# Optimization experiments

Measured on AMD Instinct MI355X. Metric: run time of the kernel, lower is better.

The kernel has to match this reference:

```python
import jax, jax.numpy as jnp
import numpy as np

EMBED_DIM = 2048
NUM_HEADS = 32
NUM_KV_HEADS = 8
HEAD_DIM = EMBED_DIM // NUM_HEADS  # 64
KV_DIM = NUM_KV_HEADS * HEAD_DIM   # 512


def setup_inputs() -> dict:
    key = jax.random.key(0)
    ks = jax.random.split(key, 5)
    B, S = 2, 2048
    scale = 0.02
    x = jax.random.normal(ks[0], (B, S, EMBED_DIM), dtype=jnp.float32)
    Wq = jax.random.normal(ks[1], (EMBED_DIM, EMBED_DIM), dtype=jnp.float32) * scale
    Wk = jax.random.normal(ks[2], (EMBED_DIM, KV_DIM), dtype=jnp.float32) * scale
    Wv = jax.random.normal(ks[3], (EMBED_DIM, KV_DIM), dtype=jnp.float32) * scale
    Wo = jax.random.normal(ks[4], (EMBED_DIM, EMBED_DIM), dtype=jnp.float32) * scale
    return {"x": x, "Wq": Wq, "Wk": Wk, "Wv": Wv, "Wo": Wo}


def reference(x, Wq, Wk, Wv, Wo):
    B, S, _ = x.shape
    g = NUM_HEADS // NUM_KV_HEADS  # queries per kv head
    # projections -> [B, H, S, D]
    q = (x @ Wq).reshape(B, S, NUM_HEADS, HEAD_DIM).transpose(0, 2, 1, 3)
    k = (x @ Wk).reshape(B, S, NUM_KV_HEADS, HEAD_DIM).transpose(0, 2, 1, 3)
    v = (x @ Wv).reshape(B, S, NUM_KV_HEADS, HEAD_DIM).transpose(0, 2, 1, 3)
    # GQA repeat_interleave on head dim
    k = jnp.repeat(k, g, axis=1)
    v = jnp.repeat(v, g, axis=1)
    scores = jnp.einsum('bhqd,bhkd->bhqk', q, k) / np.sqrt(HEAD_DIM).astype(np.float32)
    causal = jnp.tril(jnp.ones((S, S), dtype=bool))
    scores = jnp.where(causal, scores, jnp.finfo(x.dtype).min)
    attn = jax.nn.softmax(scores, axis=-1)
    out = jnp.einsum('bhqk,bhkd->bhqd', attn, v)  # [B, H, S, D]
    out = out.transpose(0, 2, 1, 3).reshape(B, S, EMBED_DIM)
    return out @ Wo
```

## Files before the change

### kernel.cpp

```cpp
#include <hip/hip_runtime.h>
#include <hip/hip_bf16.h>
#include <cstdint>
#include <type_traits>

#define EMBED 2048
#define SLEN 2048
#define NB 2
#define NHEADS 32
#define HDIM 64
#define KVDIM 512
#define MTOT (NB * SLEN)
#define NQKV (EMBED + 2 * KVDIM)

typedef __attribute__((ext_vector_type(8))) __bf16 bf16x8;
typedef __attribute__((ext_vector_type(4))) float f32x4;
typedef __attribute__((ext_vector_type(16))) float f32x16;

#define QSCALE 0.18033688011112042f

__device__ __forceinline__ ushort f2bf(float f) {
    union { float f; uint32_t u; } v; v.f = f;
    uint32_t r = (v.u + 0x7FFFu + ((v.u >> 16) & 1u)) >> 16;
    return (ushort)r;
}

__device__ __forceinline__ void gload_lds16(const ushort* g, ushort* l) {
    __builtin_amdgcn_global_load_lds(
        (const __attribute__((address_space(1))) void*)g,
        (__attribute__((address_space(3))) void*)l, 16, 0, 0);
}

__global__ __launch_bounds__(256) void k_prep(const float* __restrict__ x,
                                              const float* __restrict__ Wq,
                                              const float* __restrict__ Wk,
                                              const float* __restrict__ Wv,
                                              const float* __restrict__ Wo,
                                              ushort* __restrict__ xb,
                                              ushort* __restrict__ wt,
                                              ushort* __restrict__ wot) {
    const int tid = threadIdx.x;
    int bid = blockIdx.x;
    if (bid < 8192) {
        int i = bid * 256 + tid;
        float4 v = *(const float4*)(x + (size_t)i * 4);
        ushort4 o;
        o.x = f2bf(v.x); o.y = f2bf(v.y); o.z = f2bf(v.z); o.w = f2bf(v.w);
        *(ushort4*)(xb + (size_t)i * 4) = o;
        return;
    }
    bid -= 8192;
    const float* W; ushort* Wt; int N; float scale; int bx, by;
    if (bid < 4096)      { W = Wq; Wt = wt;                                   N = EMBED; scale = QSCALE; bx = bid & 63; by = bid >> 6; }
    else if (bid < 5120) { W = Wk; Wt = wt + (size_t)EMBED * EMBED;           N = KVDIM; scale = 1.f; int b2 = bid - 4096; bx = b2 & 15; by = b2 >> 4; }
    else if (bid < 6144) { W = Wv; Wt = wt + (size_t)(EMBED + KVDIM) * EMBED; N = KVDIM; scale = 1.f; int b2 = bid - 5120; bx = b2 & 15; by = b2 >> 4; }
    else                 { W = Wo; Wt = wot;                                  N = EMBED; scale = 1.f; int b2 = bid - 6144; bx = b2 & 63; by = b2 >> 6; }
    const int K = EMBED;
    __shared__ float tile[32][33];
    const int tx = tid & 31, ty = tid >> 5;
    const int xcol = bx * 32 + tx;
    const int y0 = by * 32;
    #pragma unroll
    for (int i = ty; i < 32; i += 8)
        tile[i][tx] = W[(size_t)(y0 + i) * N + xcol];
    __syncthreads();
    const int xo = y0 + tx;
    const int yo0 = bx * 32;
    #pragma unroll
    for (int i = ty; i < 32; i += 8)
        Wt[(size_t)(yo0 + i) * K + xo] = f2bf(tile[tx][i] * scale);
}

__global__ __launch_bounds__(256) void k_gemm_qkv2(const ushort* __restrict__ A,
                                                   const ushort* __restrict__ WtAll,
                                                   ushort* __restrict__ Qb,
                                                   ushort* __restrict__ Kb,
                                                   ushort* __restrict__ VT) {
    __shared__ alignas(16) ushort As[2][128 * 64];
    __shared__ alignas(16) ushort Bs[2][128 * 64];

    const int tid = threadIdx.x;
    const int lane = tid & 63;
    const int w = tid >> 6;
    const int wr = w >> 1, wc = w & 1;
    const int l15 = lane & 15, g = lane >> 4;
    const int K = EMBED;
    const int bid = blockIdx.x;

    if (bid < 512) {
        int f = (bid & 7) * 64 + (bid >> 3);
        const int bx = f % (EMBED / 128), by = f / (EMBED / 128);
        const int n0 = bx * 128, m0 = by * 128;
        const ushort* Bt = WtAll;

        f32x4 acc[4][4] = {};
        const ushort* pA[4];
        const ushort* pB[4];
        #pragma unroll
        for (int t = 0; t < 4; t++) {
            const int c = tid + 256 * t;
            const int r = c >> 3, gr = c & 7;
            const int sg = gr ^ (r & 7);
            pA[t] = A + (size_t)(m0 + r) * K + sg * 8;
            pB[t] = Bt + (size_t)(n0 + r) * K + sg * 8;
        }
        #pragma unroll
        for (int t = 0; t < 4; t++) {
            gload_lds16(pA[t], &As[0][(tid + 256 * t) * 8]);
            gload_lds16(pB[t], &Bs[0][(tid + 256 * t) * 8]);
        }
        __syncthreads();

        int cur = 0;
        for (int k0 = 0; k0 < K; k0 += 64) {
            if (k0 + 64 < K) {
                #pragma unroll
                for (int t = 0; t < 4; t++) {
                    gload_lds16(pA[t] + k0 + 64, &As[cur ^ 1][(tid + 256 * t) * 8]);
                    gload_lds16(pB[t] + k0 + 64, &Bs[cur ^ 1][(tid + 256 * t) * 8]);
                }
            }
            #pragma unroll
            for (int kk = 0; kk < 2; kk++) {
                bf16x8 a[4], b[4];
                #pragma unroll
                for (int i = 0; i < 4; i++)
                    a[i] = *(const bf16x8*)&As[cur][(wr * 64 + i * 16 + l15) * 64 +
                                                    (((4 * kk + g) ^ (l15 & 7)) << 3)];
                #pragma unroll
                for (int j = 0; j < 4; j++)
                    b[j] = *(const bf16x8*)&Bs[cur][(wc * 64 + j * 16 + l15) * 64 +
                                                    (((4 * kk + g) ^ (l15 & 7)) << 3)];
                #pragma unroll
                for (int i = 0; i < 4; i++)
                    #pragma unroll
                    for (int j = 0; j < 4; j++)
                        acc[i][j] = __builtin_amdgcn_mfma_f32_16x16x32_bf16(a[i], b[j], acc[i][j], 0, 0, 0);
            }
            __syncthreads();
            cur ^= 1;
        }
        #pragma unroll
        for (int i = 0; i < 4; i++)
            #pragma unroll
            for (int j = 0; j < 4; j++) {
                const int row = m0 + wr * 64 + i * 16 + g * 4;
                const int col = n0 + wc * 64 + j * 16 + l15;
                #pragma unroll
                for (int r = 0; r < 4; r++)
                    Qb[(size_t)(row + r) * EMBED + col] = f2bf(acc[i][j][r]);
            }
    } else {
        int f0 = bid - 512;
        int f = (f0 & 7) * 64 + (f0 >> 3);
        const int bx = f % 8, by = f / 8;
        const int n0 = bx * 128, m0 = by * 64;
        const ushort* Bt = WtAll + (size_t)EMBED * EMBED;

        f32x4 acc[2][4] = {};
        const ushort* pA[2];
        const ushort* pB[4];
        #pragma unroll
        for (int t = 0; t < 2; t++) {
            const int c = tid + 256 * t;
            const int r = c >> 3, gr = c & 7;
            const int sg = gr ^ (r & 7);
            pA[t] = A + (size_t)(m0 + r) * K + sg * 8;
        }
        #pragma unroll
        for (int t = 0; t < 4; t++) {
            const int c = tid + 256 * t;
            const int r = c >> 3, gr = c & 7;
            const int sg = gr ^ (r & 7);
            pB[t] = Bt + (size_t)(n0 + r) * K + sg * 8;
        }
        #pragma unroll
        for (int t = 0; t < 2; t++)
            gload_lds16(pA[t], &As[0][(tid + 256 * t) * 8]);
        #pragma unroll
        for (int t = 0; t < 4; t++)
            gload_lds16(pB[t], &Bs[0][(tid + 256 * t) * 8]);
        __syncthreads();

        int cur = 0;
        for (int k0 = 0; k0 < K; k0 += 64) {
            if (k0 + 64 < K) {
                #pragma unroll
                for (int t = 0; t < 2; t++)
                    gload_lds16(pA[t] + k0 + 64, &As[cur ^ 1][(tid + 256 * t) * 8]);
                #pragma unroll
                for (int t = 0; t < 4; t++)
                    gload_lds16(pB[t] + k0 + 64, &Bs[cur ^ 1][(tid + 256 * t) * 8]);
            }
            #pragma unroll
            for (int kk = 0; kk < 2; kk++) {
                bf16x8 a[2], b[4];
                #pragma unroll
                for (int i = 0; i < 2; i++)
                    a[i] = *(const bf16x8*)&As[cur][(wr * 32 + i * 16 + l15) * 64 +
                                                    (((4 * kk + g) ^ (l15 & 7)) << 3)];
                #pragma unroll
                for (int j = 0; j < 4; j++)
                    b[j] = *(const bf16x8*)&Bs[cur][(wc * 64 + j * 16 + l15) * 64 +
                                                    (((4 * kk + g) ^ (l15 & 7)) << 3)];
                #pragma unroll
                for (int i = 0; i < 2; i++)
                    #pragma unroll
                    for (int j = 0; j < 4; j++)
                        acc[i][j] = __builtin_amdgcn_mfma_f32_16x16x32_bf16(a[i], b[j], acc[i][j], 0, 0, 0);
            }
            __syncthreads();
            cur ^= 1;
        }

        if (n0 < KVDIM) {
            #pragma unroll
            for (int i = 0; i < 2; i++)
                #pragma unroll
                for (int j = 0; j < 4; j++) {
                    const int row = m0 + wr * 32 + i * 16 + g * 4;
                    const int col = n0 + wc * 64 + j * 16 + l15;
                    #pragma unroll
                    for (int r = 0; r < 4; r++)
                        Kb[(size_t)(row + r) * KVDIM + col] = f2bf(acc[i][j][r]);
                }
        } else {
            ushort* TT = &Bs[0][0];
            #pragma unroll
            for (int i = 0; i < 2; i++)
                #pragma unroll
                for (int j = 0; j < 4; j++) {
                    const int rowL = wr * 32 + i * 16 + g * 4;
                    const int colL = wc * 64 + j * 16 + l15;
                    #pragma unroll
                    for (int r = 0; r < 4; r++)
                        TT[colL * 72 + rowL + r] = f2bf(acc[i][j][r]);
                }
            __syncthreads();
            const int c = tid >> 1, half = tid & 1;
            const ushort* src = TT + c * 72 + half * 32;
            ushort* dst = VT + (size_t)(n0 - KVDIM + c) * MTOT + m0 + half * 32;
            #pragma unroll
            for (int q = 0; q < 4; q++)
                *(uint4*)(dst + q * 8) = *(const uint4*)(src + q * 8);
        }
    }
}

template <typename OUT_T>
__global__ __launch_bounds__(256) void k_gemm_bt(const ushort* __restrict__ A,
                                                 const ushort* __restrict__ Bt,
                                                 OUT_T* __restrict__ C,
                                                 int M, int N, int K) {
    __shared__ alignas(16) ushort As[2][128 * 64];
    __shared__ alignas(16) ushort Bs[2][128 * 64];

    const int tid = threadIdx.x;
    const int lane = tid & 63;
    const int w = tid >> 6;
    const int wr = w >> 1, wc = w & 1;
    const int l15 = lane & 15, g = lane >> 4;
    const int nwg = (N / 128) * (M / 128);
    int f = blockIdx.y * (N / 128) + blockIdx.x;
    f = (f & 7) * (nwg >> 3) + (f >> 3);
    const int n0 = (f % (N / 128)) * 128;
    const int m0 = (f / (N / 128)) * 128;

    f32x4 acc[4][4] = {};

    const ushort* pA[4];
    const ushort* pB[4];
    #pragma unroll
    for (int t = 0; t < 4; t++) {
        const int c = tid + 256 * t;
        const int r = c >> 3, gr = c & 7;
        const int sg = gr ^ (r & 7);
        pA[t] = A + (size_t)(m0 + r) * K + sg * 8;
        pB[t] = Bt + (size_t)(n0 + r) * K + sg * 8;
    }

    #pragma unroll
    for (int t = 0; t < 4; t++) {
        gload_lds16(pA[t], &As[0][(tid + 256 * t) * 8]);
        gload_lds16(pB[t], &Bs[0][(tid + 256 * t) * 8]);
    }
    __syncthreads();

    int cur = 0;
    for (int k0 = 0; k0 < K; k0 += 64) {
        if (k0 + 64 < K) {
            #pragma unroll
            for (int t = 0; t < 4; t++) {
                gload_lds16(pA[t] + k0 + 64, &As[cur ^ 1][(tid + 256 * t) * 8]);
                gload_lds16(pB[t] + k0 + 64, &Bs[cur ^ 1][(tid + 256 * t) * 8]);
            }
        }
        #pragma unroll
        for (int kk = 0; kk < 2; kk++) {
            bf16x8 a[4], b[4];
            #pragma unroll
            for (int i = 0; i < 4; i++)
                a[i] = *(const bf16x8*)&As[cur][(wr * 64 + i * 16 + l15) * 64 +
                                                (((4 * kk + g) ^ (l15 & 7)) << 3)];
            #pragma unroll
            for (int j = 0; j < 4; j++)
                b[j] = *(const bf16x8*)&Bs[cur][(wc * 64 + j * 16 + l15) * 64 +
                                                (((4 * kk + g) ^ (l15 & 7)) << 3)];
            #pragma unroll
            for (int i = 0; i < 4; i++)
                #pragma unroll
                for (int j = 0; j < 4; j++)
                    acc[i][j] = __builtin_amdgcn_mfma_f32_16x16x32_bf16(a[i], b[j], acc[i][j], 0, 0, 0);
        }
        __syncthreads();
        cur ^= 1;
    }

    #pragma unroll
    for (int i = 0; i < 4; i++) {
        #pragma unroll
        for (int j = 0; j < 4; j++) {
            const int row = m0 + wr * 64 + i * 16 + g * 4;
            const int col = n0 + wc * 64 + j * 16 + l15;
            #pragma unroll
            for (int r = 0; r < 4; r++) {
                float val = acc[i][j][r];
                if constexpr (std::is_same<OUT_T, ushort>::value)
                    C[(size_t)(row + r) * N + col] = f2bf(val);
                else
                    C[(size_t)(row + r) * N + col] = val;
            }
        }
    }
}

__global__ __launch_bounds__(512, 4) void k_attn(const ushort* __restrict__ Qg,
                                                 const ushort* __restrict__ Kg,
                                                 const ushort* __restrict__ VTg,
                                                 ushort* __restrict__ Og) {
    __shared__ alignas(16) ushort Ks[2][64 * 64];
    __shared__ alignas(16) ushort Vs[2][64 * 64];

    const int tid = threadIdx.x;
    const int lane = tid & 63;
    const int wq = tid >> 6;
    const int l31 = lane & 31;
    const int hi = lane >> 5;

    const int flat = blockIdx.x + (blockIdx.y << 3) + (blockIdx.z << 8);
    const int lo = flat & 255, hv = flat >> 8;
    const int bi = hv ? (7 - (lo & 7)) : (lo & 7);
    const int h = lo >> 3;
    const int b = hv;
    const int kh = h >> 2;
    const size_t rowbase = (size_t)b * SLEN;

    const int q0 = bi * 256;
    const int qw0 = q0 + wq * 32;
    const int nt = (q0 >> 6) + 4;

    bf16x8 qf[4];
    {
        const ushort* qrow = Qg + (rowbase + qw0 + l31) * EMBED + h * HDIM;
        #pragma unroll
        for (int s = 0; s < 4; s++)
            qf[s] = *(const bf16x8*)(qrow + s * 16 + hi * 8);
    }

    union { uint32_t u[4]; bf16x8 v; } onesf;
    onesf.u[0] = 0x3F803F80u; onesf.u[1] = 0x3F803F80u;
    onesf.u[2] = 0x3F803F80u; onesf.u[3] = 0x3F803F80u;

    const int srow = tid >> 3;
    const int sgr = tid & 7;
    const int woff = srow * 64 + ((sgr ^ (srow & 7)) << 3);
    const ushort* kgbase = Kg + (rowbase + srow) * KVDIM + kh * HDIM + sgr * 8;
    const ushort* vgbase = VTg + (size_t)(kh * HDIM + srow) * MTOT + b * SLEN + sgr * 8;

    {
        uint4 kr = *(const uint4*)kgbase;
        uint4 vr = *(const uint4*)vgbase;
        *(uint4*)&Ks[0][woff] = kr;
        *(uint4*)&Vs[0][woff] = vr;
    }
    __syncthreads();

    f32x16 oacc[2], lacc;
    #pragma unroll
    for (int d = 0; d < 2; d++)
        #pragma unroll
        for (int r = 0; r < 16; r++) oacc[d][r] = 0.f;
    #pragma unroll
    for (int r = 0; r < 16; r++) lacc[r] = 0.f;

    int cur = 0;
    for (int kt = 0; kt < nt; ++kt) {
        const int k0 = kt * 64;
        const bool pref = (kt + 1 < nt);
        uint4 kr, vr;
        if (pref) {
            kr = *(const uint4*)(kgbase + (size_t)(k0 + 64) * KVDIM);
            vr = *(const uint4*)(vgbase + k0 + 64);
        }

        if (k0 <= qw0 + 31) {
            f32x16 sacc[2];
            #pragma unroll
            for (int st = 0; st < 2; st++)
                #pragma unroll
                for (int r = 0; r < 16; r++) sacc[st][r] = 0.f;
            __builtin_amdgcn_s_setprio(1);
            #pragma unroll
            for (int st = 0; st < 2; st++) {
                const int krow = st * 32 + l31;
                #pragma unroll
                for (int s = 0; s < 4; s++) {
                    bf16x8 af = *(const bf16x8*)&Ks[cur][krow * 64 + (((2 * s + hi) ^ (l31 & 7)) << 3)];
                    sacc[st] = __builtin_amdgcn_mfma_f32_32x32x16_bf16(af, qf[s], sacc[st], 0, 0, 0);
                }
            }
            __builtin_amdgcn_s_setprio(0);
            if (k0 + 63 > qw0) {
                const int q = qw0 + l31;
                #pragma unroll
                for (int st = 0; st < 2; st++)
                    #pragma unroll
                    for (int r = 0; r < 16; r++) {
                        int kpos = k0 + st * 32 + (r & 3) + 8 * (r >> 2) + 4 * hi;
                        if (kpos > q) sacc[st][r] = -1e30f;
                    }
            }
            #pragma unroll
            for (int st = 0; st < 2; st++)
                #pragma unroll
                for (int r = 0; r < 16; r++)
                    sacc[st][r] = __builtin_amdgcn_exp2f(sacc[st][r]);
            uint32_t pr[2][8];
            #pragma unroll
            for (int st = 0; st < 2; st++)
                #pragma unroll
                for (int k = 0; k < 8; k++) {
                    uint32_t d;
                    asm("v_cvt_pk_bf16_f32 %0, %1, %2"
                        : "=v"(d) : "v"(sacc[st][2 * k]), "v"(sacc[st][2 * k + 1]));
                    pr[st][k] = d;
                }
            #pragma unroll
            for (int c = 0; c < 2; c++) {
                #pragma unroll
                for (int tt = 0; tt < 2; tt++) {
                    const int pb = 4 * tt;
                    uint32_t w0 = pr[c][pb + 0], w2 = pr[c][pb + 2];
                    uint32_t w1 = pr[c][pb + 1], w3 = pr[c][pb + 3];
                    asm("v_permlane32_swap_b32 %0, %1" : "+v"(w0), "+v"(w2));
                    asm("v_permlane32_swap_b32 %0, %1" : "+v"(w1), "+v"(w3));
                    union { uint32_t u[4]; bf16x8 v; } pf;
                    pf.u[0] = w0; pf.u[1] = w1; pf.u[2] = w2; pf.u[3] = w3;
                    const int t = 2 * c + tt;
                    __builtin_amdgcn_s_setprio(1);
                    lacc = __builtin_amdgcn_mfma_f32_32x32x16_bf16(pf.v, onesf.v, lacc, 0, 0, 0);
                    #pragma unroll
                    for (int dt = 0; dt < 2; dt++) {
                        const int vrow = dt * 32 + l31;
                        bf16x8 vf = *(const bf16x8*)&Vs[cur][vrow * 64 + (((2 * t + hi) ^ (l31 & 7)) << 3)];
                        oacc[dt] = __builtin_amdgcn_mfma_f32_32x32x16_bf16(pf.v, vf, oacc[dt], 0, 0, 0);
                    }
                    __builtin_amdgcn_s_setprio(0);
                }
            }
        }

        if (pref) {
            *(uint4*)&Ks[cur ^ 1][woff] = kr;
            *(uint4*)&Vs[cur ^ 1][woff] = vr;
        }
        __syncthreads();
        cur ^= 1;
    }

    #pragma unroll
    for (int r = 0; r < 16; r++) {
        const int rr = (r & 3) + 8 * (r >> 2) + 4 * hi;
        float inv = 1.f / lacc[r];
        const size_t base = (rowbase + qw0 + rr) * EMBED + h * HDIM;
        Og[base + l31] = f2bf(oacc[0][r] * inv);
        Og[base + 32 + l31] = f2bf(oacc[1][r] * inv);
    }
}

#define WS_XB  ((size_t)0)
#define WS_QB  (WS_XB + (size_t)MTOT * EMBED)
#define WS_KB  (WS_QB + (size_t)MTOT * EMBED)
#define WS_VT  (WS_KB + (size_t)MTOT * KVDIM)
#define WS_WT  (WS_VT + (size_t)KVDIM * MTOT)
#define WS_WOT (WS_WT + (size_t)NQKV * EMBED)

extern "C" void kernel_launch(void* const* d_in, const int* in_sizes, int n_in,
                              void* d_out, int out_size, void* d_ws, size_t ws_size,
                              hipStream_t stream) {
    const float* x  = (const float*)d_in[0];
    const float* Wq = (const float*)d_in[1];
    const float* Wk = (const float*)d_in[2];
    const float* Wv = (const float*)d_in[3];
    const float* Wo = (const float*)d_in[4];
    float* out = (float*)d_out;
    ushort* ws = (ushort*)d_ws;

    k_prep<<<18432, 256, 0, stream>>>(x, Wq, Wk, Wv, Wo,
                                      ws + WS_XB, ws + WS_WT, ws + WS_WOT);

    k_gemm_qkv2<<<1024, 256, 0, stream>>>(
        ws + WS_XB, ws + WS_WT, ws + WS_QB, ws + WS_KB, ws + WS_VT);

    k_attn<<<dim3(8, 32, 2), 512, 0, stream>>>(
        ws + WS_QB, ws + WS_KB, ws + WS_VT, ws + WS_XB);

    k_gemm_bt<float><<<dim3(EMBED / 128, MTOT / 128), 256, 0, stream>>>(
        ws + WS_XB, ws + WS_WOT, out, MTOT, EMBED, EMBED);
}
```

Measured before the change: 184.2 us.

## Replace double-buffered BK=64 swizzled QKV GEMM loop with single-buffered BK=32

Rewrites the QKV projection GEMM main loop to use a single LDS buffer with K-step 32 and no XOR swizzle, syncing before and after each global-to-LDS load. It also gives the V transpose its own dedicated shared buffer. This cuts LDS use, which may raise occupancy, but it removes the load/compute overlap, doubles the number of barriers, and unswizzled 64-byte row strides may cause LDS bank conflicts.

```diff
diff --git a/kernel.cpp b/kernel.cpp
--- a/kernel.cpp
+++ b/kernel.cpp
@@ -75,8 +75,9 @@
                                                    ushort* __restrict__ Qb,
                                                    ushort* __restrict__ Kb,
                                                    ushort* __restrict__ VT) {
-    __shared__ alignas(16) ushort As[2][128 * 64];
-    __shared__ alignas(16) ushort Bs[2][128 * 64];
+    __shared__ alignas(16) ushort As[128 * 32];
+    __shared__ alignas(16) ushort Bs[128 * 32];
+    __shared__ alignas(16) ushort TT[128 * 72];
 
     const int tid = threadIdx.x;
     const int lane = tid & 63;
@@ -93,51 +94,36 @@
         const ushort* Bt = WtAll;
 
         f32x4 acc[4][4] = {};
-        const ushort* pA[4];
-        const ushort* pB[4];
-        #pragma unroll
-        for (int t = 0; t < 4; t++) {
-            const int c = tid + 256 * t;
-            const int r = c >> 3, gr = c & 7;
-            const int sg = gr ^ (r & 7);
-            pA[t] = A + (size_t)(m0 + r) * K + sg * 8;
-            pB[t] = Bt + (size_t)(n0 + r) * K + sg * 8;
-        }
-        #pragma unroll
-        for (int t = 0; t < 4; t++) {
-            gload_lds16(pA[t], &As[0][(tid + 256 * t) * 8]);
-            gload_lds16(pB[t], &Bs[0][(tid + 256 * t) * 8]);
-        }
-        __syncthreads();
-
-        int cur = 0;
-        for (int k0 = 0; k0 < K; k0 += 64) {
-            if (k0 + 64 < K) {
-                #pragma unroll
-                for (int t = 0; t < 4; t++) {
-                    gload_lds16(pA[t] + k0 + 64, &As[cur ^ 1][(tid + 256 * t) * 8]);
-                    gload_lds16(pB[t] + k0 + 64, &Bs[cur ^ 1][(tid + 256 * t) * 8]);
-                }
-            }
-            #pragma unroll
-            for (int kk = 0; kk < 2; kk++) {
-                bf16x8 a[4], b[4];
-                #pragma unroll
-                for (int i = 0; i < 4; i++)
-                    a[i] = *(const bf16x8*)&As[cur][(wr * 64 + i * 16 + l15) * 64 +
-                                                    (((4 * kk + g) ^ (l15 & 7)) << 3)];
+
+        const int c0 = tid, c1 = tid + 256;
+        const int rA0 = c0 >> 2, sA0 = c0 & 3;
+        const int rA1 = c1 >> 2, sA1 = c1 & 3;
+
+        const ushort* pA0 = A + (size_t)(m0 + rA0) * K + sA0 * 8;
+        const ushort* pA1 = A + (size_t)(m0 + rA1) * K + sA1 * 8;
+        const ushort* pB0 = Bt + (size_t)(n0 + rA0) * K + sA0 * 8;
+        const ushort* pB1 = Bt + (size_t)(n0 + rA1) * K + sA1 * 8;
+
+        for (int k0 = 0; k0 < K; k0 += 32) {
+            __syncthreads();
+            gload_lds16(pA0 + k0, As + c0 * 8);
+            gload_lds16(pA1 + k0, As + c1 * 8);
+            gload_lds16(pB0 + k0, Bs + c0 * 8);
+            gload_lds16(pB1 + k0, Bs + c1 * 8);
+            __syncthreads();
+
+            bf16x8 a[4], b[4];
+            #pragma unroll
+            for (int i = 0; i < 4; i++)
+                a[i] = *(const bf16x8*)&As[(wr * 64 + i * 16 + l15) * 32 + 8 * g];
+            #pragma unroll
+            for (int j = 0; j < 4; j++)
+                b[j] = *(const bf16x8*)&Bs[(wc * 64 + j * 16 + l15) * 32 + 8 * g];
+            #pragma unroll
+            for (int i = 0; i < 4; i++)
                 #pragma unroll
                 for (int j = 0; j < 4; j++)
-                    b[j] = *(const bf16x8*)&Bs[cur][(wc * 64 + j * 16 + l15) * 64 +
-                                                    (((4 * kk + g) ^ (l15 & 7)) << 3)];
-                #pragma unroll
-                for (int i = 0; i < 4; i++)
-                    #pragma unroll
-                    for (int j = 0; j < 4; j++)
-                        acc[i][j] = __builtin_amdgcn_mfma_f32_16x16x32_bf16(a[i], b[j], acc[i][j], 0, 0, 0);
-            }
-            __syncthreads();
-            cur ^= 1;
+                    acc[i][j] = __builtin_amdgcn_mfma_f32_16x16x32_bf16(a[i], b[j], acc[i][j], 0, 0, 0);
         }
         #pragma unroll
         for (int i = 0; i < 4; i++)
@@ -157,59 +143,36 @@
         const ushort* Bt = WtAll + (size_t)EMBED * EMBED;
 
         f32x4 acc[2][4] = {};
-        const ushort* pA[2];
-        const ushort* pB[4];
-        #pragma unroll
-        for (int t = 0; t < 2; t++) {
-            const int c = tid + 256 * t;
-            const int r = c >> 3, gr = c & 7;
-            const int sg = gr ^ (r & 7);
-            pA[t] = A + (size_t)(m0 + r) * K + sg * 8;
-        }
-        #pragma unroll
-        for (int t = 0; t < 4; t++) {
-            const int c = tid + 256 * t;
-            const int r = c >> 3, gr = c & 7;
-            const int sg = gr ^ (r & 7);
-            pB[t] = Bt + (size_t)(n0 + r) * K + sg * 8;
-        }
-        #pragma unroll
-        for (int t = 0; t < 2; t++)
-            gload_lds16(pA[t], &As[0][(tid + 256 * t) * 8]);
-        #pragma unroll
-        for (int t = 0; t < 4; t++)
-            gload_lds16(pB[t], &Bs[0][(tid + 256 * t) * 8]);
-        __syncthreads();
-
-        int cur = 0;
-        for (int k0 = 0; k0 < K; k0 += 64) {
-            if (k0 + 64 < K) {
-                #pragma unroll
-                for (int t = 0; t < 2; t++)
-                    gload_lds16(pA[t] + k0 + 64, &As[cur ^ 1][(tid + 256 * t) * 8]);
-                #pragma unroll
-                for (int t = 0; t < 4; t++)
-                    gload_lds16(pB[t] + k0 + 64, &Bs[cur ^ 1][(tid + 256 * t) * 8]);
-            }
-            #pragma unroll
-            for (int kk = 0; kk < 2; kk++) {
-                bf16x8 a[2], b[4];
-                #pragma unroll
-                for (int i = 0; i < 2; i++)
-                    a[i] = *(const bf16x8*)&As[cur][(wr * 32 + i * 16 + l15) * 64 +
-                                                    (((4 * kk + g) ^ (l15 & 7)) << 3)];
+
+        const int c0 = tid, c1 = tid + 256;
+        const int rA0 = c0 >> 2, sA0 = c0 & 3;
+        const int rB0 = c0 >> 2, sB0 = c0 & 3;
+        const int rB1 = c1 >> 2, sB1 = c1 & 3;
+
+        const ushort* pA0 = A + (size_t)(m0 + rA0) * K + sA0 * 8;
+        const ushort* pB0 = Bt + (size_t)(n0 + rB0) * K + sB0 * 8;
+        const ushort* pB1 = Bt + (size_t)(n0 + rB1) * K + sB1 * 8;
+
+        for (int k0 = 0; k0 < K; k0 += 32) {
+            __syncthreads();
+            if (tid < 256) {  }
+            gload_lds16(pA0 + k0, As + c0 * 8);
+            gload_lds16(pB0 + k0, Bs + c0 * 8);
+            gload_lds16(pB1 + k0, Bs + c1 * 8);
+            __syncthreads();
+
+            bf16x8 a[2], b[4];
+            #pragma unroll
+            for (int i = 0; i < 2; i++)
+                a[i] = *(const bf16x8*)&As[(wr * 32 + i * 16 + l15) * 32 + 8 * g];
+            #pragma unroll
+            for (int j = 0; j < 4; j++)
+                b[j] = *(const bf16x8*)&Bs[(wc * 64 + j * 16 + l15) * 32 + 8 * g];
+            #pragma unroll
+            for (int i = 0; i < 2; i++)
                 #pragma unroll
                 for (int j = 0; j < 4; j++)
-                    b[j] = *(const bf16x8*)&Bs[cur][(wc * 64 + j * 16 + l15) * 64 +
-                                                    (((4 * kk + g) ^ (l15 & 7)) << 3)];
-                #pragma unroll
-                for (int i = 0; i < 2; i++)
-                    #pragma unroll
-                    for (int j = 0; j < 4; j++)
-                        acc[i][j] = __builtin_amdgcn_mfma_f32_16x16x32_bf16(a[i], b[j], acc[i][j], 0, 0, 0);
-            }
-            __syncthreads();
-            cur ^= 1;
+                    acc[i][j] = __builtin_amdgcn_mfma_f32_16x16x32_bf16(a[i], b[j], acc[i][j], 0, 0, 0);
         }
 
         if (n0 < KVDIM) {
@@ -224,7 +187,6 @@
                         Kb[(size_t)(row + r) * KVDIM + col] = f2bf(acc[i][j][r]);
                 }
         } else {
-            ushort* TT = &Bs[0][0];
             #pragma unroll
             for (int i = 0; i < 2; i++)
                 #pragma unroll
```

Result: slower. 196.2 us (+6.5%).
